# Performance work log

Measured on AMD Instinct MI355X. Metric: run time of the kernel, lower is better.

The kernel has to match this reference:

```python
import jax, jax.numpy as jnp
import numpy as np

BETA_MIN, BETA_MAX = 0.01, 0.995
EPS_DELTA, EPS_RMS = 1e-6, 1e-5


def _rmsnorm(x, w):
    ms = jnp.mean(x * x, axis=-1, keepdims=True)
    return x * jax.lax.rsqrt(ms + EPS_RMS) * w


def _delta_scan(q, k, v, beta, mask, bb1, bb2):
    # q, k, v: [B, S, D]; beta, mask: [B, S, 1]; bb1, bb2: scalars
    phi_q = jax.nn.elu(q) + 1.0
    phi_k = jax.nn.elu(k) + 1.0
    b1_base = jnp.clip(jax.nn.sigmoid(bb1), BETA_MIN, BETA_MAX)
    b2_base = jnp.clip(jax.nn.sigmoid(bb2), BETA_MIN, BETA_MAX)
    B, S, D = q.shape

    def step(carry, inp):
        H1, H2, Z1, Z2 = carry
        qt, kt, vt, bt, mt = inp  # qt/kt/vt: [B,D], bt/mt: [B,1]
        bin_t = jnp.clip(bt, BETA_MIN, BETA_MAX)
        b1 = jnp.clip(b1_base * bin_t, BETA_MIN, BETA_MAX)  # [B,1]
        b2 = jnp.clip(b2_base * bin_t, BETA_MIN, BETA_MAX)
        kv = jnp.einsum('bd,be->bde', kt, vt) * mt[:, :, None]  # [B,D,D]
        H1 = H1 * b1[:, :, None] + kv
        H2 = H2 * b2[:, :, None] + kv
        km = kt * mt
        Z1 = Z1 * b1 + km
        Z2 = Z2 * b2 + km
        num = jnp.einsum('bd,bde->be', qt, H1 + H2)
        den = jnp.maximum(jnp.sum(qt * (Z1 + Z2), axis=-1, keepdims=True), EPS_DELTA)
        return (H1, H2, Z1, Z2), num / den * mt

    init = (jnp.zeros((B, D, D), q.dtype), jnp.zeros((B, D, D), q.dtype),
            jnp.zeros((B, D), q.dtype), jnp.zeros((B, D), q.dtype))
    xs = tuple(a.swapaxes(0, 1) for a in (phi_q, phi_k, v, beta, mask))
    _, outs = jax.lax.scan(step, init, xs)
    return outs.swapaxes(0, 1)  # [B, S, D]


def setup_inputs() -> dict:
    key = jax.random.key(0)
    B, S, Dm, H = 4, 2048, 512, 8
    ks = jax.random.split(key, 8)
    scale = float(1.0 / np.sqrt(Dm))
    return {
        'x': jax.random.normal(ks[0], (B, S, Dm), jnp.float32),
        'mask': jnp.ones((B, S), jnp.float32),
        'Wq': jax.random.normal(ks[1], (Dm, Dm), jnp.float32) * scale,
        'Wk': jax.random.normal(ks[2], (Dm, Dm), jnp.float32) * scale,
        'Wv': jax.random.normal(ks[3], (Dm, Dm), jnp.float32) * scale,
        'Wb': jax.random.normal(ks[4], (H, Dm), jnp.float32) * scale,
        'bb': jnp.full((H,), 1.5, jnp.float32),
        'Wo': jax.random.normal(ks[5], (Dm, Dm), jnp.float32) * scale,
        'bo': jnp.zeros((Dm,), jnp.float32),
        'ln_w': jnp.ones((Dm,), jnp.float32),
        'recency': jnp.zeros((H,), jnp.float32),
        'base_beta_1': jnp.asarray(2.0, jnp.float32),
        'base_beta_2': jnp.asarray(3.0, jnp.float32),
    }


def reference(x, mask, Wq, Wk, Wv, Wb, bb, Wo, bo, ln_w, recency,
              base_beta_1, base_beta_2):
    B, S, Dm = x.shape
    H = recency.shape[0]
    d = Dm // H
    h = _rmsnorm(x, ln_w)
    q = h @ Wq.T
    k = h @ Wk.T
    v = h @ Wv.T
    # input-conditioned gate with per-head recency bias  -> [B, S, H]
    beta = jax.nn.sigmoid(h @ Wb.T + bb + recency)

    def to_heads(t):  # [B,S,Dm] -> [B*H, S, d]
        return t.reshape(B, S, H, d).transpose(0, 2, 1, 3).reshape(B * H, S, d)

    qh, kh, vh = to_heads(q), to_heads(k), to_heads(v)
    betah = beta.transpose(0, 2, 1).reshape(B * H, S, 1)
    maskh = jnp.broadcast_to(mask[:, None, :, None], (B, H, S, 1)).reshape(B * H, S, 1)
    o = _delta_scan(qh, kh, vh, betah, maskh, base_beta_1, base_beta_2)
    o = o.reshape(B, H, S, d).transpose(0, 2, 1, 3).reshape(B, S, Dm)
    return x + (o @ Wo.T + bo)
```

## Files before the change

### kernel.cpp

```cpp
#include <hip/hip_runtime.h>
#include <stdint.h>

typedef unsigned short u16;
typedef short bf16x8 __attribute__((ext_vector_type(8)));
typedef unsigned short u16x8 __attribute__((ext_vector_type(8)));
typedef unsigned short u16x4 __attribute__((ext_vector_type(4)));
typedef float f32x4 __attribute__((ext_vector_type(4)));

#define S_ 2048
#define DM 512
#define DH 64
#define CL 64
#define NCH 32

#define SW(r, sc) ((r) * 72 + ((sc) ^ (((r) & 7) << 3)))

__device__ __forceinline__ float b2f(u16 u) { return __uint_as_float(((unsigned)u) << 16); }
__device__ __forceinline__ u16 f2b(float f) {
    unsigned v = __float_as_uint(f);
    unsigned r = v + 0x7fffu + ((v >> 16) & 1u);
    return (u16)(r >> 16);
}
__device__ __forceinline__ float phi_elu(float x) { return x > 0.f ? x + 1.f : __expf(x); }
__device__ __forceinline__ float clip01(float v) { return fminf(fmaxf(v, 0.01f), 0.995f); }

__device__ __forceinline__ void gload16(const u16* g, u16* l) {
    __builtin_amdgcn_global_load_lds((const __attribute__((address_space(1))) void*)g,
                                     (__attribute__((address_space(3))) void*)l, 16, 0, 0);
}

__global__ __launch_bounds__(256) void k_rbw(const float* __restrict__ x, const float* __restrict__ lnw,
                                             const float* __restrict__ Wb, const float* __restrict__ bb,
                                             const float* __restrict__ rec, const float* __restrict__ bb1p,
                                             const float* __restrict__ bb2p, u16* __restrict__ h,
                                             float* __restrict__ lb1, float* __restrict__ lb2,
                                             const float* __restrict__ Wq, const float* __restrict__ Wk,
                                             const float* __restrict__ Wv, const float* __restrict__ Wo,
                                             u16* __restrict__ wcat, u16* __restrict__ wo) {
    if (blockIdx.x >= 2048) {
        int idx = (blockIdx.x - 2048) * 256 + threadIdx.x;
        int e0 = idx << 2;
        if (e0 < 1536 * 512) {
            int r = e0 >> 9, ccol = e0 & 511;
            const float* src = (r < 512) ? (Wq + (size_t)r * 512)
                             : (r < 1024) ? (Wk + (size_t)(r - 512) * 512)
                                          : (Wv + (size_t)(r - 1024) * 512);
            float4 v = *(const float4*)(src + ccol);
            u16x4 o = {f2b(v.x), f2b(v.y), f2b(v.z), f2b(v.w)};
            *(u16x4*)(wcat + e0) = o;
        } else {
            int e = e0 - 1536 * 512;
            float4 v = *(const float4*)(Wo + e);
            u16x4 o = {f2b(v.x), f2b(v.y), f2b(v.z), f2b(v.w)};
            *(u16x4*)(wo + e) = o;
        }
        return;
    }
    int wave = threadIdx.x >> 6, lane = threadIdx.x & 63;
    int row = blockIdx.x * 4 + wave;
    const float* xr = x + (size_t)row * DM + lane * 8;
    float4 v0 = *(const float4*)xr;
    float4 v1 = *(const float4*)(xr + 4);
    float ss = v0.x * v0.x + v0.y * v0.y + v0.z * v0.z + v0.w * v0.w +
               v1.x * v1.x + v1.y * v1.y + v1.z * v1.z + v1.w * v1.w;
    #pragma unroll
    for (int off = 32; off; off >>= 1) ss += __shfl_xor(ss, off, 64);
    float sc = rsqrtf(ss * (1.f / DM) + 1e-5f);
    const float* wr_ = lnw + lane * 8;
    float4 w0 = *(const float4*)wr_;
    float4 w1 = *(const float4*)(wr_ + 4);
    float hv[8];
    hv[0] = v0.x * sc * w0.x; hv[1] = v0.y * sc * w0.y;
    hv[2] = v0.z * sc * w0.z; hv[3] = v0.w * sc * w0.w;
    hv[4] = v1.x * sc * w1.x; hv[5] = v1.y * sc * w1.y;
    hv[6] = v1.z * sc * w1.z; hv[7] = v1.w * sc * w1.w;
    u16x8 o;
    #pragma unroll
    for (int j = 0; j < 8; j++) o[j] = f2b(hv[j]);
    *(u16x8*)(h + (size_t)row * DM + lane * 8) = o;
    float acc[8];
    #pragma unroll
    for (int hd = 0; hd < 8; hd++) {
        const float* wp = Wb + hd * DM + lane * 8;
        float4 a0 = *(const float4*)wp;
        float4 a1 = *(const float4*)(wp + 4);
        acc[hd] = hv[0] * a0.x + hv[1] * a0.y + hv[2] * a0.z + hv[3] * a0.w +
                  hv[4] * a1.x + hv[5] * a1.y + hv[6] * a1.z + hv[7] * a1.w;
    }
    #pragma unroll
    for (int hd = 0; hd < 8; hd++) {
        #pragma unroll
        for (int off = 32; off; off >>= 1) acc[hd] += __shfl_xor(acc[hd], off, 64);
    }
    if (lane == 0) {
        float b1b = clip01(1.f / (1.f + __expf(-bb1p[0])));
        float b2b = clip01(1.f / (1.f + __expf(-bb2p[0])));
        int b = row >> 11, s = row & 2047;
        #pragma unroll
        for (int hd = 0; hd < 8; hd++) {
            float logit = acc[hd] + bb[hd] + rec[hd];
            float beta = 1.f / (1.f + __expf(-logit));
            float bin = clip01(beta);
            float b1 = clip01(b1b * bin);
            float b2 = clip01(b2b * bin);
            size_t o2 = (size_t)((b << 3) + hd) * S_ + s;
            lb1[o2] = log2f(b1);
            lb2[o2] = log2f(b2);
        }
    }
}

template<int MODE, int NT>
__global__ __launch_bounds__(256) void k_gemm(const u16* __restrict__ A, const u16* __restrict__ Bw, int K,
                                              const float* __restrict__ mask, u16* __restrict__ qh,
                                              u16* __restrict__ kh, u16* __restrict__ vh,
                                              const float* __restrict__ xres, const float* __restrict__ bo,
                                              float* __restrict__ outp) {
    __shared__ u16 SH[16384];
    u16* As = SH;
    u16* Bs = SH + 8192;
    int tid = threadIdx.x;
    int lane = tid & 63, w = tid >> 6;
    int wr = w >> 1, wc = w & 1;
    int hwid = blockIdx.y * gridDim.x + blockIdx.x;
    int nwg = gridDim.x * NT;
    int q8 = nwg >> 3;
    int logical = (hwid & 7) * q8 + (hwid >> 3);
    int mTile = logical / NT, nTile = logical % NT;
    int m0 = mTile * 128, n0 = nTile * 128;
    f32x4 acc[4][4] = {};
    int r0 = tid >> 3;
    int swc8 = ((lane & 7) ^ (lane >> 3)) << 3;
    const u16* gA0 = A + (size_t)(m0 + r0) * K + swc8;
    const u16* gB0 = Bw + (size_t)(n0 + r0) * K + swc8;
    u16* lA = As + w * 512;
    u16* lB = Bs + w * 512;
    int l15 = lane & 15;
    int kgrp = lane >> 4;
    for (int k0 = 0; k0 < K; k0 += 64) {
        if (k0) __syncthreads();
        #pragma unroll
        for (int rb = 0; rb < 4; rb++) {
            gload16(gA0 + (size_t)rb * 32 * K + k0, lA + rb * 2048);
            gload16(gB0 + (size_t)rb * 32 * K + k0, lB + rb * 2048);
        }
        __syncthreads();
        #pragma unroll
        for (int kk = 0; kk < 2; kk++) {
            int kg = kgrp + kk * 4;
            int cg = (kg ^ (l15 & 7)) << 3;
            bf16x8 af[4], bfr[4];
            #pragma unroll
            for (int m = 0; m < 4; m++) af[m] = *(const bf16x8*)&As[(wr * 64 + m * 16 + l15) * 64 + cg];
            #pragma unroll
            for (int n = 0; n < 4; n++) bfr[n] = *(const bf16x8*)&Bs[(wc * 64 + n * 16 + l15) * 64 + cg];
            #pragma unroll
            for (int m = 0; m < 4; m++)
                #pragma unroll
                for (int n = 0; n < 4; n++)
                    acc[m][n] = __builtin_amdgcn_mfma_f32_16x16x32_bf16(af[m], bfr[n], acc[m][n], 0, 0, 0);
        }
    }
    __syncthreads();
    if constexpr (MODE == 0) {
        int mat = n0 >> 9;
        int cb = n0 & 511;
        u16* basep = (mat == 0) ? qh : (mat == 1) ? kh : vh;
        #pragma unroll
        for (int P = 0; P < 2; P++) {
            if (wr == P) {
                #pragma unroll
                for (int m = 0; m < 4; m++)
                    #pragma unroll
                    for (int n = 0; n < 4; n++)
                        #pragma unroll
                        for (int r = 0; r < 4; r++) {
                            int rl = m * 16 + ((lane >> 4) << 2) + r;
                            int colL = wc * 64 + n * 16 + l15;
                            SH[rl * 140 + colL] = f2b(acc[m][n][r]);
                        }
            }
            __syncthreads();
            {
                int rl = tid >> 2;
                int gr = m0 + P * 64 + rl;
                int b = gr >> 11, s = gr & 2047;
                float mv = (mat == 1) ? mask[(b << 11) + s] : 1.f;
                #pragma unroll
                for (int cc = 0; cc < 4; cc++) {
                    int cl = ((tid & 3) << 5) + (cc << 3);
                    u16x8 vv = *(const u16x8*)&SH[rl * 140 + cl];
                    int f = cb + cl;
                    int hh = f >> 6, j = f & 63;
                    u16* dst = basep + ((size_t)(b * 8 + hh) * S_ + s) * DH + j;
                    if (mat == 2) {
                        *(u16x8*)dst = vv;
                    } else {
                        u16x8 ov;
                        #pragma unroll
                        for (int e = 0; e < 8; e++) {
                            float v = b2f(vv[e]);
                            ov[e] = f2b(phi_elu(v) * mv);
                        }
                        *(u16x8*)dst = ov;
                    }
                }
            }
            __syncthreads();
        }
    } else {
        float* SF = (float*)SH;
        #pragma unroll
        for (int Pq = 0; Pq < 4; Pq++) {
            if (wr == (Pq >> 1)) {
                int mbase = (Pq & 1) * 2;
                #pragma unroll
                for (int mm = 0; mm < 2; mm++)
                    #pragma unroll
                    for (int n = 0; n < 4; n++)
                        #pragma unroll
                        for (int r = 0; r < 4; r++) {
                            int rl = mm * 16 + ((lane >> 4) << 2) + r;
                            int colL = wc * 64 + n * 16 + l15;
                            SF[rl * 136 + colL] = acc[mbase + mm][n][r];
                        }
            }
            __syncthreads();
            {
                int rl = tid >> 3;
                int gr = m0 + Pq * 32 + rl;
                int col0 = (tid & 7) << 4;
                const float* xr = xres + (size_t)gr * DM + n0 + col0;
                float* orow = outp + (size_t)gr * DM + n0 + col0;
                #pragma unroll
                for (int cc = 0; cc < 4; cc++) {
                    int cl = col0 + (cc << 2);
                    float4 v = *(const float4*)&SF[rl * 136 + cl];
                    float4 xv = *(const float4*)(xr + (cc << 2));
                    float4 bv = *(const float4*)(bo + n0 + cl);
                    float4 ov = {v.x + xv.x + bv.x, v.y + xv.y + bv.y,
                                 v.z + xv.z + bv.z, v.w + xv.w + bv.w};
                    *(float4*)(orow + (cc << 2)) = ov;
                }
            }
            __syncthreads();
        }
    }
}

__global__ __launch_bounds__(256) void k_pass1(const u16* __restrict__ kh, const u16* __restrict__ vh,
                                               const float* __restrict__ lb1, const float* __restrict__ lb2,
                                               u16* __restrict__ S1b, u16* __restrict__ S2b,
                                               float* __restrict__ z1, float* __restrict__ z2,
                                               float* __restrict__ P1, float* __restrict__ P2) {
    __shared__ u16 Kw1[64 * 72];
    __shared__ u16 Kw2[64 * 72];
    __shared__ u16 Vt[64 * 72];
    __shared__ float Ls1[64], Ls2[64];
    int tid = threadIdx.x;
    int bh = blockIdx.x >> 5, c = blockIdx.x & 31;
    int wave = tid >> 6, lane = tid & 63;
    size_t base = ((size_t)bh * S_ + c * CL) * DH;
    if (wave == 0) {
        float v = lb1[(size_t)bh * S_ + c * CL + lane];
        #pragma unroll
        for (int d = 1; d < 64; d <<= 1) { float o = __shfl_up(v, d, 64); if (lane >= d) v += o; }
        Ls1[lane] = v;
    } else if (wave == 1) {
        float v = lb2[(size_t)bh * S_ + c * CL + lane];
        #pragma unroll
        for (int d = 1; d < 64; d <<= 1) { float o = __shfl_up(v, d, 64); if (lane >= d) v += o; }
        Ls2[lane] = v;
    }
    int ss = tid & 63, i0 = (tid >> 6) << 4;
    const u16* kr = kh + base + (size_t)ss * DH + i0;
    u16x8 kk0 = *(const u16x8*)kr;
    u16x8 kk1 = *(const u16x8*)(kr + 8);
    {
        const u16* vr = vh + base + (size_t)ss * DH + i0;
        u16x8 vv0 = *(const u16x8*)vr;
        u16x8 vv1 = *(const u16x8*)(vr + 8);
        #pragma unroll
        for (int j = 0; j < 8; j++) {
            Vt[SW(i0 + j, ss)] = vv0[j];
            Vt[SW(i0 + 8 + j, ss)] = vv1[j];
        }
    }
    __syncthreads();
    float w1 = exp2f(Ls1[63] - Ls1[ss]);
    float w2 = exp2f(Ls2[63] - Ls2[ss]);
    #pragma unroll
    for (int j = 0; j < 8; j++) {
        float k0 = b2f(kk0[j]), k1 = b2f(kk1[j]);
        Kw1[SW(i0 + j, ss)] = f2b(w1 * k0);
        Kw2[SW(i0 + j, ss)] = f2b(w2 * k0);
        Kw1[SW(i0 + 8 + j, ss)] = f2b(w1 * k1);
        Kw2[SW(i0 + 8 + j, ss)] = f2b(w2 * k1);
    }
    if (tid == 0) { P1[blockIdx.x] = exp2f(Ls1[63]); P2[blockIdx.x] = exp2f(Ls2[63]); }
    __syncthreads();
    int l15 = lane & 15, kh8 = (lane >> 4) << 3;
    int j0 = wave << 4;
    bf16x8 vf0 = *(const bf16x8*)&Vt[SW(j0 + l15, kh8)];
    bf16x8 vf1 = *(const bf16x8*)&Vt[SW(j0 + l15, 32 + kh8)];
    f32x4 a1[4], a2[4];
    #pragma unroll
    for (int it = 0; it < 4; it++) { a1[it] = (f32x4){0,0,0,0}; a2[it] = (f32x4){0,0,0,0}; }
    #pragma unroll
    for (int it = 0; it < 4; it++) {
        int ir = (it << 4) + l15;
        bf16x8 b0 = *(const bf16x8*)&Kw1[SW(ir, kh8)];
        bf16x8 b1 = *(const bf16x8*)&Kw1[SW(ir, 32 + kh8)];
        a1[it] = __builtin_amdgcn_mfma_f32_16x16x32_bf16(vf0, b0, a1[it], 0, 0, 0);
        a1[it] = __builtin_amdgcn_mfma_f32_16x16x32_bf16(vf1, b1, a1[it], 0, 0, 0);
        bf16x8 c0 = *(const bf16x8*)&Kw2[SW(ir, kh8)];
        bf16x8 c1 = *(const bf16x8*)&Kw2[SW(ir, 32 + kh8)];
        a2[it] = __builtin_amdgcn_mfma_f32_16x16x32_bf16(vf0, c0, a2[it], 0, 0, 0);
        a2[it] = __builtin_amdgcn_mfma_f32_16x16x32_bf16(vf1, c1, a2[it], 0, 0, 0);
    }
    {
        int iz = tid >> 2, sg = tid & 3;
        u16x8 x0 = *(const u16x8*)&Kw1[SW(iz, sg << 4)];
        u16x8 x1 = *(const u16x8*)&Kw1[SW(iz, (sg << 4) + 8)];
        u16x8 y0 = *(const u16x8*)&Kw2[SW(iz, sg << 4)];
        u16x8 y1 = *(const u16x8*)&Kw2[SW(iz, (sg << 4) + 8)];
        float z1v = 0.f, z2v = 0.f;
        #pragma unroll
        for (int j = 0; j < 8; j++) {
            z1v += b2f(x0[j]) + b2f(x1[j]);
            z2v += b2f(y0[j]) + b2f(y1[j]);
        }
        z1v += __shfl_xor(z1v, 1, 64); z1v += __shfl_xor(z1v, 2, 64);
        z2v += __shfl_xor(z2v, 1, 64); z2v += __shfl_xor(z2v, 2, 64);
        if (sg == 0) {
            z1[(size_t)blockIdx.x * 64 + iz] = z1v;
            z2[(size_t)blockIdx.x * 64 + iz] = z2v;
        }
    }
    int jr0 = j0 + ((lane >> 4) << 2);
    size_t so = (size_t)blockIdx.x * 4096;
    #pragma unroll
    for (int it = 0; it < 4; it++) {
        int ii = (it << 4) + l15;
        #pragma unroll
        for (int r = 0; r < 4; r++) {
            S1b[so + (size_t)(jr0 + r) * 64 + ii] = f2b(a1[it][r]);
            S2b[so + (size_t)(jr0 + r) * 64 + ii] = f2b(a2[it][r]);
        }
    }
}

__global__ __launch_bounds__(256) void k_pass2(u16* __restrict__ S1b, u16* __restrict__ S2b,
                                               float* __restrict__ z1, float* __restrict__ z2,
                                               const float* __restrict__ P1, const float* __restrict__ P2) {
    int blk = blockIdx.x;
    if (blk < 512) {
        int bh = blk >> 4;
        int e = ((blk & 15) << 8) + threadIdx.x;
        float c1 = 0.f, c2 = 0.f;
        #pragma unroll 4
        for (int c = 0; c < NCH; c++) {
            int bc = bh * NCH + c;
            size_t idx = (size_t)bc * 4096 + e;
            float p1 = P1[bc], p2 = P2[bc];
            float t1 = b2f(S1b[idx]); S1b[idx] = f2b(c1); c1 = c1 * p1 + t1;
            float t2 = b2f(S2b[idx]); S2b[idx] = f2b(c2); c2 = c2 * p2 + t2;
        }
    } else {
        int bh = ((blk - 512) << 2) + (threadIdx.x >> 6);
        int e = threadIdx.x & 63;
        float y1 = 0.f, y2 = 0.f;
        #pragma unroll 4
        for (int c = 0; c < NCH; c++) {
            int bc = bh * NCH + c;
            size_t zi = (size_t)bc * 64 + e;
            float p1 = P1[bc], p2 = P2[bc];
            float t1 = z1[zi]; z1[zi] = y1; y1 = y1 * p1 + t1;
            float t2 = z2[zi]; z2[zi] = y2; y2 = y2 * p2 + t2;
        }
    }
}

__global__ __launch_bounds__(256) void k_pass3(const u16* __restrict__ qh, const u16* __restrict__ kh,
                                               const u16* __restrict__ vh, const float* __restrict__ lb1,
                                               const float* __restrict__ lb2, const u16* __restrict__ S1b,
                                               const u16* __restrict__ S2b, const float* __restrict__ z1,
                                               const float* __restrict__ z2, const float* __restrict__ mask,
                                               u16* __restrict__ obf) {
    __shared__ u16 Vt[64 * 72];
    __shared__ u16 AWs[64 * 72];
    __shared__ float Ls1[64], Ls2[64], dens[64], qZ1[64], qZ2[64];
    int tid = threadIdx.x;
    int bh = blockIdx.x >> 5, c = blockIdx.x & 31;
    int wave = tid >> 6, lane = tid & 63;
    size_t base = ((size_t)bh * S_ + c * CL) * DH;
    if (wave == 0) {
        float v = lb1[(size_t)bh * S_ + c * CL + lane];
        #pragma unroll
        for (int d = 1; d < 64; d <<= 1) { float o = __shfl_up(v, d, 64); if (lane >= d) v += o; }
        Ls1[lane] = v;
    } else if (wave == 1) {
        float v = lb2[(size_t)bh * S_ + c * CL + lane];
        #pragma unroll
        for (int d = 1; d < 64; d <<= 1) { float o = __shfl_up(v, d, 64); if (lane >= d) v += o; }
        Ls2[lane] = v;
    }
    {
        int ss = tid & 63, i0 = (tid >> 6) << 4;
        const u16* vr = vh + base + (size_t)ss * DH + i0;
        u16x8 vv0 = *(const u16x8*)vr;
        u16x8 vv1 = *(const u16x8*)(vr + 8);
        #pragma unroll
        for (int j = 0; j < 8; j++) {
            Vt[SW(i0 + j, ss)] = vv0[j];
            Vt[SW(i0 + 8 + j, ss)] = vv1[j];
        }
    }
    {
        int t = tid >> 2, g = tid & 3;
        const u16* qp = qh + base + (size_t)t * DH + (g << 4);
        u16x8 q0 = *(const u16x8*)qp;
        u16x8 q1 = *(const u16x8*)(qp + 8);
        const float* z1p = z1 + (size_t)blockIdx.x * 64 + (g << 4);
        const float* z2p = z2 + (size_t)blockIdx.x * 64 + (g << 4);
        float az1 = 0.f, az2 = 0.f;
        #pragma unroll
        for (int m = 0; m < 8; m++) {
            float qv0 = b2f(q0[m]), qv1 = b2f(q1[m]);
            az1 += qv0 * z1p[m] + qv1 * z1p[m + 8];
            az2 += qv0 * z2p[m] + qv1 * z2p[m + 8];
        }
        az1 += __shfl_xor(az1, 1, 64); az1 += __shfl_xor(az1, 2, 64);
        az2 += __shfl_xor(az2, 1, 64); az2 += __shfl_xor(az2, 2, 64);
        if (g == 0) { qZ1[t] = az1; qZ2[t] = az2; }
    }
    int l15 = lane & 15, kh8 = (lane >> 4) << 3;
    int t0 = wave << 4;
    const u16* qb = qh + base + (size_t)(t0 + l15) * DH;
    bf16x8 qf0 = *(const bf16x8*)(qb + kh8);
    bf16x8 qf1 = *(const bf16x8*)(qb + 32 + kh8);
    f32x4 accA[4];
    #pragma unroll
    for (int st = 0; st < 4; st++) accA[st] = (f32x4){0, 0, 0, 0};
    #pragma unroll
    for (int st = 0; st < 4; st++) {
        const u16* kb = kh + base + (size_t)((st << 4) + l15) * DH;
        bf16x8 kf0 = *(const bf16x8*)(kb + kh8);
        bf16x8 kf1 = *(const bf16x8*)(kb + 32 + kh8);
        accA[st] = __builtin_amdgcn_mfma_f32_16x16x32_bf16(qf0, kf0, accA[st], 0, 0, 0);
        accA[st] = __builtin_amdgcn_mfma_f32_16x16x32_bf16(qf1, kf1, accA[st], 0, 0, 0);
    }
    __syncthreads();
    int trow = t0 + ((lane >> 4) << 2);
    float l1t[4], l2t[4];
    #pragma unroll
    for (int r = 0; r < 4; r++) { l1t[r] = Ls1[trow + r]; l2t[r] = Ls2[trow + r]; }
    float rs[4] = {0.f, 0.f, 0.f, 0.f};
    #pragma unroll
    for (int st = 0; st < 4; st++) {
        int s = (st << 4) + l15;
        float s1 = Ls1[s], s2 = Ls2[s];
        #pragma unroll
        for (int r = 0; r < 4; r++) {
            float w = 0.f;
            if (s <= trow + r) w = exp2f(l1t[r] - s1) + exp2f(l2t[r] - s2);
            u16 awb = f2b(accA[st][r] * w);
            AWs[SW(trow + r, s)] = awb;
            rs[r] += b2f(awb);
        }
    }
    #pragma unroll
    for (int off = 1; off < 16; off <<= 1) {
        #pragma unroll
        for (int r = 0; r < 4; r++) rs[r] += __shfl_xor(rs[r], off, 64);
    }
    if (l15 == 0) {
        #pragma unroll
        for (int r = 0; r < 4; r++) dens[trow + r] = rs[r];
    }
    __syncthreads();
    bf16x8 awf0 = *(const bf16x8*)&AWs[SW(t0 + l15, kh8)];
    bf16x8 awf1 = *(const bf16x8*)&AWs[SW(t0 + l15, 32 + kh8)];
    const u16* h1g = S1b + (size_t)blockIdx.x * 4096;
    const u16* h2g = S2b + (size_t)blockIdx.x * 4096;
    f32x4 accO[4], accC1[4], accC2[4];
    #pragma unroll
    for (int jt = 0; jt < 4; jt++) {
        accO[jt] = (f32x4){0, 0, 0, 0};
        accC1[jt] = (f32x4){0, 0, 0, 0};
        accC2[jt] = (f32x4){0, 0, 0, 0};
    }
    #pragma unroll
    for (int jt = 0; jt < 4; jt++) {
        int jr = (jt << 4) + l15;
        bf16x8 v0 = *(const bf16x8*)&Vt[SW(jr, kh8)];
        bf16x8 v1 = *(const bf16x8*)&Vt[SW(jr, 32 + kh8)];
        accO[jt] = __builtin_amdgcn_mfma_f32_16x16x32_bf16(awf0, v0, accO[jt], 0, 0, 0);
        accO[jt] = __builtin_amdgcn_mfma_f32_16x16x32_bf16(awf1, v1, accO[jt], 0, 0, 0);
        bf16x8 h10 = *(const bf16x8*)(h1g + (size_t)jr * 64 + kh8);
        bf16x8 h11 = *(const bf16x8*)(h1g + (size_t)jr * 64 + 32 + kh8);
        accC1[jt] = __builtin_amdgcn_mfma_f32_16x16x32_bf16(qf0, h10, accC1[jt], 0, 0, 0);
        accC1[jt] = __builtin_amdgcn_mfma_f32_16x16x32_bf16(qf1, h11, accC1[jt], 0, 0, 0);
        bf16x8 h20 = *(const bf16x8*)(h2g + (size_t)jr * 64 + kh8);
        bf16x8 h21 = *(const bf16x8*)(h2g + (size_t)jr * 64 + 32 + kh8);
        accC2[jt] = __builtin_amdgcn_mfma_f32_16x16x32_bf16(qf0, h20, accC2[jt], 0, 0, 0);
        accC2[jt] = __builtin_amdgcn_mfma_f32_16x16x32_bf16(qf1, h21, accC2[jt], 0, 0, 0);
    }
    int b = bh >> 3, hh = bh & 7;
    #pragma unroll
    for (int r = 0; r < 4; r++) {
        int t = trow + r;
        float e1 = exp2f(l1t[r]), e2 = exp2f(l2t[r]);
        float den = dens[t] + e1 * qZ1[t] + e2 * qZ2[t];
        den = fmaxf(den, 1e-6f);
        int sg = (c << 6) + t;
        float mv = mask[(size_t)b * S_ + sg];
        float inv = mv / den;
        u16* op = obf + ((size_t)b * S_ + sg) * DM + hh * DH;
        #pragma unroll
        for (int jt = 0; jt < 4; jt++) {
            float numv = accO[jt][r] + e1 * accC1[jt][r] + e2 * accC2[jt][r];
            op[(jt << 4) + l15] = f2b(numv * inv);
        }
    }
}

extern "C" void kernel_launch(void* const* d_in, const int* in_sizes, int n_in,
                              void* d_out, int out_size, void* d_ws, size_t ws_size,
                              hipStream_t stream) {
    const float* x    = (const float*)d_in[0];
    const float* mask = (const float*)d_in[1];
    const float* Wq   = (const float*)d_in[2];
    const float* Wk   = (const float*)d_in[3];
    const float* Wv   = (const float*)d_in[4];
    const float* Wb   = (const float*)d_in[5];
    const float* bb   = (const float*)d_in[6];
    const float* Wo   = (const float*)d_in[7];
    const float* bo   = (const float*)d_in[8];
    const float* lnw  = (const float*)d_in[9];
    const float* rec  = (const float*)d_in[10];
    const float* bb1  = (const float*)d_in[11];
    const float* bb2  = (const float*)d_in[12];
    float* out = (float*)d_out;

    char* w = (char*)d_ws;
    u16* h    = (u16*)w;  w += (size_t)8192 * 512 * 2;
    u16* wcat = (u16*)w;  w += (size_t)1536 * 512 * 2;
    u16* wo   = (u16*)w;  w += (size_t)512 * 512 * 2;
    u16* qh   = (u16*)w;  w += (size_t)8192 * 512 * 2;
    u16* kh   = (u16*)w;  w += (size_t)8192 * 512 * 2;
    u16* vh   = (u16*)w;  w += (size_t)8192 * 512 * 2;
    float* lb1 = (float*)w; w += (size_t)32 * 2048 * 4;
    float* lb2 = (float*)w; w += (size_t)32 * 2048 * 4;
    u16* S1b  = (u16*)w;  w += (size_t)1024 * 4096 * 2;
    u16* S2b  = (u16*)w;  w += (size_t)1024 * 4096 * 2;
    float* z1  = (float*)w; w += (size_t)1024 * 64 * 4;
    float* z2  = (float*)w; w += (size_t)1024 * 64 * 4;
    float* P1  = (float*)w; w += 4096;
    float* P2  = (float*)w; w += 4096;
    u16* obf   = (u16*)w;   w += (size_t)8192 * 512 * 2;

    k_rbw<<<3072, 256, 0, stream>>>(x, lnw, Wb, bb, rec, bb1, bb2, h, lb1, lb2,
                                    Wq, Wk, Wv, Wo, wcat, wo);
    k_gemm<0, 12><<<dim3(64, 12), 256, 0, stream>>>(h, wcat, 512, mask, qh, kh, vh, nullptr, nullptr, nullptr);
    k_pass1<<<1024, 256, 0, stream>>>(kh, vh, lb1, lb2, S1b, S2b, z1, z2, P1, P2);
    k_pass2<<<520, 256, 0, stream>>>(S1b, S2b, z1, z2, P1, P2);
    k_pass3<<<1024, 256, 0, stream>>>(qh, kh, vh, lb1, lb2, S1b, S2b, z1, z2, mask, obf);
    k_gemm<1, 4><<<dim3(64, 4), 256, 0, stream>>>(obf, wo, 512, nullptr, nullptr, nullptr, nullptr, x, bo, out);
}
```

Before: 99.67 us.

## Stage scan outputs through LDS for vector stores and remap blocks across XCDs

Pass1 and pass3 now write their MFMA accumulator tiles into shared memory first, then emit 16-byte vectorized global stores instead of scattered 2-byte stores. Block indices in pass1, pass2 and pass3 are remapped so that consecutive chunks of the same head land on the same XCD (the blockIdx & 7 interleave), which is meant to improve L2 locality for the inter-pass state buffers. The cost is extra barriers and LDS round trips.

```diff
diff --git a/kernel.cpp b/kernel.cpp
--- a/kernel.cpp
+++ b/kernel.cpp
@@ -258,7 +258,8 @@
     __shared__ u16 Vt[64 * 72];
     __shared__ float Ls1[64], Ls2[64];
     int tid = threadIdx.x;
-    int bh = blockIdx.x >> 5, c = blockIdx.x & 31;
+    int blkL = ((blockIdx.x & 7) << 7) + (blockIdx.x >> 3);
+    int bh = blkL >> 5, c = blkL & 31;
     int wave = tid >> 6, lane = tid & 63;
     size_t base = ((size_t)bh * S_ + c * CL) * DH;
     if (wave == 0) {
@@ -297,7 +298,7 @@
         Kw1[SW(i0 + 8 + j, ss)] = f2b(w1 * k1);
         Kw2[SW(i0 + 8 + j, ss)] = f2b(w2 * k1);
     }
-    if (tid == 0) { P1[blockIdx.x] = exp2f(Ls1[63]); P2[blockIdx.x] = exp2f(Ls2[63]); }
+    if (tid == 0) { P1[blkL] = exp2f(Ls1[63]); P2[blkL] = exp2f(Ls2[63]); }
     __syncthreads();
     int l15 = lane & 15, kh8 = (lane >> 4) << 3;
     int j0 = wave << 4;
@@ -333,20 +334,29 @@
         z1v += __shfl_xor(z1v, 1, 64); z1v += __shfl_xor(z1v, 2, 64);
         z2v += __shfl_xor(z2v, 1, 64); z2v += __shfl_xor(z2v, 2, 64);
         if (sg == 0) {
-            z1[(size_t)blockIdx.x * 64 + iz] = z1v;
-            z2[(size_t)blockIdx.x * 64 + iz] = z2v;
-        }
-    }
+            z1[(size_t)blkL * 64 + iz] = z1v;
+            z2[(size_t)blkL * 64 + iz] = z2v;
+        }
+    }
+    __syncthreads();
     int jr0 = j0 + ((lane >> 4) << 2);
-    size_t so = (size_t)blockIdx.x * 4096;
     #pragma unroll
     for (int it = 0; it < 4; it++) {
         int ii = (it << 4) + l15;
         #pragma unroll
         for (int r = 0; r < 4; r++) {
-            S1b[so + (size_t)(jr0 + r) * 64 + ii] = f2b(a1[it][r]);
-            S2b[so + (size_t)(jr0 + r) * 64 + ii] = f2b(a2[it][r]);
-        }
+            Vt[SW(jr0 + r, ii)] = f2b(a1[it][r]);
+            Kw1[SW(jr0 + r, ii)] = f2b(a2[it][r]);
+        }
+    }
+    __syncthreads();
+    {
+        int row = tid >> 2, c16 = (tid & 3) << 4;
+        size_t so = (size_t)blkL * 4096 + (size_t)row * 64 + c16;
+        *(u16x8*)&S1b[so]     = *(const u16x8*)&Vt[SW(row, c16)];
+        *(u16x8*)&S1b[so + 8] = *(const u16x8*)&Vt[SW(row, c16 + 8)];
+        *(u16x8*)&S2b[so]     = *(const u16x8*)&Kw1[SW(row, c16)];
+        *(u16x8*)&S2b[so + 8] = *(const u16x8*)&Kw1[SW(row, c16 + 8)];
     }
 }
 
@@ -355,8 +365,10 @@
                                                const float* __restrict__ P1, const float* __restrict__ P2) {
     int blk = blockIdx.x;
     if (blk < 512) {
-        int bh = blk >> 4;
-        int e = ((blk & 15) << 8) + threadIdx.x;
+        int xx = blk & 7, j = blk >> 3;
+        int bh = (xx << 2) + (j >> 4);
+        int part = j & 15;
+        int e = (part << 8) + threadIdx.x;
         float c1 = 0.f, c2 = 0.f;
         #pragma unroll 4
         for (int c = 0; c < NCH; c++) {
@@ -391,7 +403,8 @@
     __shared__ u16 AWs[64 * 72];
     __shared__ float Ls1[64], Ls2[64], dens[64], qZ1[64], qZ2[64];
     int tid = threadIdx.x;
-    int bh = blockIdx.x >> 5, c = blockIdx.x & 31;
+    int blkL = ((blockIdx.x & 7) << 7) + (blockIdx.x >> 3);
+    int bh = blkL >> 5, c = blkL & 31;
     int wave = tid >> 6, lane = tid & 63;
     size_t base = ((size_t)bh * S_ + c * CL) * DH;
     if (wave == 0) {
@@ -421,8 +434,8 @@
         const u16* qp = qh + base + (size_t)t * DH + (g << 4);
         u16x8 q0 = *(const u16x8*)qp;
         u16x8 q1 = *(const u16x8*)(qp + 8);
-        const float* z1p = z1 + (size_t)blockIdx.x * 64 + (g << 4);
-        const float* z2p = z2 + (size_t)blockIdx.x * 64 + (g << 4);
+        const float* z1p = z1 + (size_t)blkL * 64 + (g << 4);
+        const float* z2p = z2 + (size_t)blkL * 64 + (g << 4);
         float az1 = 0.f, az2 = 0.f;
         #pragma unroll
         for (int m = 0; m < 8; m++) {
@@ -481,8 +494,8 @@
     __syncthreads();
     bf16x8 awf0 = *(const bf16x8*)&AWs[SW(t0 + l15, kh8)];
     bf16x8 awf1 = *(const bf16x8*)&AWs[SW(t0 + l15, 32 + kh8)];
-    const u16* h1g = S1b + (size_t)blockIdx.x * 4096;
-    const u16* h2g = S2b + (size_t)blockIdx.x * 4096;
+    const u16* h1g = S1b + (size_t)blkL * 4096;
+    const u16* h2g = S2b + (size_t)blkL * 4096;
     f32x4 accO[4], accC1[4], accC2[4];
     #pragma unroll
     for (int jt = 0; jt < 4; jt++) {
@@ -507,6 +520,7 @@
         accC2[jt] = __builtin_amdgcn_mfma_f32_16x16x32_bf16(qf1, h21, accC2[jt], 0, 0, 0);
     }
     int b = bh >> 3, hh = bh & 7;
+    __syncthreads();
     #pragma unroll
     for (int r = 0; r < 4; r++) {
         int t = trow + r;
@@ -516,12 +530,19 @@
         int sg = (c << 6) + t;
         float mv = mask[(size_t)b * S_ + sg];
         float inv = mv / den;
-        u16* op = obf + ((size_t)b * S_ + sg) * DM + hh * DH;
         #pragma unroll
         for (int jt = 0; jt < 4; jt++) {
             float numv = accO[jt][r] + e1 * accC1[jt][r] + e2 * accC2[jt][r];
-            op[(jt << 4) + l15] = f2b(numv * inv);
-        }
+            AWs[SW(t, (jt << 4) + l15)] = f2b(numv * inv);
+        }
+    }
+    __syncthreads();
+    {
+        int row = tid >> 2, c16 = (tid & 3) << 4;
+        int sg = (c << 6) + row;
+        u16* op = obf + ((size_t)b * S_ + sg) * DM + hh * DH + c16;
+        *(u16x8*)op       = *(const u16x8*)&AWs[SW(row, c16)];
+        *(u16x8*)(op + 8) = *(const u16x8*)&AWs[SW(row, c16 + 8)];
     }
 }
 
```

Result: no change. 101.7 us (+2.0%).
